# Performance work log

Hardware: AMD Instinct MI355X
Metric: run time of the kernel (lower is better)

Reference implementation:

```python
import jax, jax.numpy as jnp
import numpy as np
from jax import lax

UNITS_OSC = 512
STEPS = 100
DT = 0.001
ACTION_DIM = 256
BATCH = 256


def complex_dense(zc, Wr, Wi, br, bi):
    # zc: [B, 2n] = concat(real, imag); complex matmul with relu on both parts
    n = Wr.shape[0]
    xr, xi = zc[:, :n], zc[:, n:]
    yr = jax.nn.relu(xr @ Wr - xi @ Wi + br)
    yi = jax.nn.relu(xr @ Wi + xi @ Wr + bi)
    return jnp.concatenate([yr, yi], axis=-1)


def hopf_step(zc, omega, mu, b):
    # zc: [B, 2*UNITS_OSC]; Hopf dynamics dz = ((mu - |z|^2) + i*k*omega) z + b, Euler step
    x, y = zc[:, :UNITS_OSC], zc[:, UNITS_OSC:]
    r2 = x * x + y * y
    w = omega * jnp.arange(1, UNITS_OSC + 1, dtype=zc.dtype)  # [B, UNITS_OSC]
    nx = x + DT * ((mu - r2) * x - w * y + b)
    ny = y + DT * ((mu - r2) * y + w * x)
    return jnp.concatenate([nx, ny], axis=-1)


def _dense_init(key, fan_in, fan_out):
    return jax.random.normal(key, (fan_in, fan_out), dtype=jnp.float32) / np.sqrt(fan_in)


def setup_inputs() -> dict:
    key = jax.random.key(0)
    ks = jax.random.split(key, 16)
    inp = {
        'motion_state': jax.random.normal(ks[0], (BATCH, 64), dtype=jnp.float32),
        'robot_state': jax.random.normal(ks[1], (BATCH, 128), dtype=jnp.float32),
        'z': 0.1 * jax.random.normal(ks[2], (BATCH, 2 * UNITS_OSC), dtype=jnp.float32),
        'W_ms': _dense_init(ks[3], 64, 256), 'b_ms': jnp.zeros((256,), jnp.float32),
        'W_rs': _dense_init(ks[4], 128, 256), 'b_rs': jnp.zeros((256,), jnp.float32),
        'W_cmb': _dense_init(ks[5], 512, 512), 'b_cmb': jnp.zeros((512,), jnp.float32),
        'W_om': _dense_init(ks[6], 512, 1), 'b_om': jnp.zeros((1,), jnp.float32),
        'W_mu': _dense_init(ks[7], 512, 512), 'b_mu': jnp.zeros((512,), jnp.float32),
        'W_b': _dense_init(ks[8], 512, 512), 'b_b': jnp.zeros((512,), jnp.float32),
        'Wr0': _dense_init(ks[9], 512, 1024), 'Wi0': _dense_init(ks[10], 512, 1024),
        'br0': jnp.zeros((1024,), jnp.float32), 'bi0': jnp.zeros((1024,), jnp.float32),
        'Wr1': _dense_init(ks[11], 1024, 512), 'Wi1': _dense_init(ks[12], 1024, 512),
        'br1': jnp.zeros((512,), jnp.float32), 'bi1': jnp.zeros((512,), jnp.float32),
        'Wr2': _dense_init(ks[13], 512, 256), 'Wi2': _dense_init(ks[14], 512, 256),
        'br2': jnp.zeros((256,), jnp.float32), 'bi2': jnp.zeros((256,), jnp.float32),
    }
    return inp


def reference(motion_state, robot_state, z,
              W_ms, b_ms, W_rs, b_rs, W_cmb, b_cmb, W_om, b_om, W_mu, b_mu, W_b, b_b,
              Wr0, Wi0, br0, bi0, Wr1, Wi1, br1, bi1, Wr2, Wi2, br2, bi2):
    # --- StateEncoder ---
    ms = jax.nn.relu(motion_state @ W_ms + b_ms)
    rs = jax.nn.relu(robot_state @ W_rs + b_rs)
    st = jax.nn.relu(jnp.concatenate([ms, rs], axis=-1) @ W_cmb + b_cmb)
    omega = jnp.abs(jax.nn.relu(st @ W_om + b_om))   # [B, 1]
    mu = jnp.abs(jax.nn.relu(st @ W_mu + b_mu))      # [B, UNITS_OSC]
    bb = jnp.abs(jax.nn.relu(st @ W_b + b_b))        # [B, UNITS_OSC]

    def mlp(zc):
        zc = complex_dense(zc, Wr0, Wi0, br0, bi0)
        zc = complex_dense(zc, Wr1, Wi1, br1, bi1)
        return complex_dense(zc, Wr2, Wi2, br2, bi2)  # [B, 2*ACTION_DIM]

    # first oscillator step (this z is the z_out returned by the original module)
    z_out = hopf_step(z, omega, mu, bb)
    o0 = mlp(z_out)

    def body(zc, _):
        zn = hopf_step(zc, omega, mu, bb)
        return zn, mlp(zn)

    _, os = lax.scan(body, z_out, None, length=STEPS - 1)   # [STEPS-1, B, 2A]
    out = jnp.concatenate([o0[None], os], axis=0)           # [STEPS, B, 2A]
    out = jnp.transpose(out, (1, 0, 2))[:, :, :ACTION_DIM]  # [B, STEPS, A]
    return out, z_out, omega, mu, bb
```

## Files before the change

### kernel.cpp

```cpp
#include <hip/hip_runtime.h>
#include <hip/hip_bf16.h>

#define STEPS 100
#define DTC 0.001f

typedef __attribute__((ext_vector_type(8))) short bf16x8;
typedef __attribute__((ext_vector_type(4))) float f32x4;

__device__ __forceinline__ void gload16(const void* g, void* l) {
  __builtin_amdgcn_global_load_lds(
      (const __attribute__((address_space(1))) void*)g,
      (__attribute__((address_space(3))) void*)l,
      16, 0, 0);
}


__global__ __launch_bounds__(512)
void front(const float* __restrict__ ms_in, const float* __restrict__ rs_in,
           const float* __restrict__ z,
           const float* __restrict__ Wms, const float* __restrict__ bms,
           const float* __restrict__ Wrs, const float* __restrict__ brs,
           const float* __restrict__ Wc, const float* __restrict__ bc,
           const float* __restrict__ Wmu, const float* __restrict__ bmu,
           const float* __restrict__ Wb, const float* __restrict__ bbias,
           const float* __restrict__ Wom, const float* __restrict__ bom,
           __hip_bfloat16* __restrict__ A0, float* __restrict__ z_out,
           float* __restrict__ om_out, float* __restrict__ mu_out,
           float* __restrict__ bb_out) {
  const int b = blockIdx.x;
  const int n = threadIdx.x;
  __shared__ float sIn[192];
  __shared__ float stA[512];
  __shared__ float stB[512];
  if (n < 64) sIn[n] = ms_in[b * 64 + n];
  else if (n < 192) sIn[n] = rs_in[b * 128 + (n - 64)];
  __syncthreads();
  float a1;
  if (n < 256) {
    a1 = bms[n];
    for (int k = 0; k < 64; ++k) a1 += sIn[k] * Wms[k * 256 + n];
  } else {
    int nn = n - 256;
    a1 = brs[nn];
    for (int k = 0; k < 128; ++k) a1 += sIn[64 + k] * Wrs[k * 256 + nn];
  }
  stA[n] = fmaxf(a1, 0.f);
  __syncthreads();
  float a2 = bc[n];
  for (int k = 0; k < 512; ++k) a2 += stA[k] * Wc[k * 512 + n];
  stB[n] = fmaxf(a2, 0.f);
  __syncthreads();
  float am = bmu[n], ab = bbias[n];
  for (int k = 0; k < 512; ++k) {
    float sv = stB[k];
    am += sv * Wmu[k * 512 + n];
    ab += sv * Wb[k * 512 + n];
  }
  const float muv = fabsf(fmaxf(am, 0.f));
  const float bbv = fabsf(fmaxf(ab, 0.f));
  mu_out[b * 512 + n] = muv;
  bb_out[b * 512 + n] = bbv;
  stA[n] = stB[n] * Wom[n];
  __syncthreads();
  for (int off = 256; off > 0; off >>= 1) {
    if (n < off) stA[n] += stA[n + off];
    __syncthreads();
  }
  const float om = fabsf(fmaxf(stA[0] + bom[0], 0.f));
  if (n == 0) om_out[b] = om;
  float x = z[b * 1024 + n];
  float y = z[b * 1024 + 512 + n];
  const float w = om * (float)(n + 1);
  for (int t = 0; t < STEPS; ++t) {
    float r2 = x * x + y * y;
    float g = muv - r2;
    float nx = x + DTC * (g * x - w * y + bbv);
    float ny = y + DTC * (g * y + w * x);
    x = nx; y = ny;
    if (t == 0) {
      z_out[b * 1024 + n] = x;
      z_out[b * 1024 + 512 + n] = y;
    }
    size_t row = (size_t)b * STEPS + t;
    A0[row * 1024 + n] = __float2bfloat16(x);
    A0[row * 1024 + 512 + n] = __float2bfloat16(y);
  }
}


__constant__ int    jSrcC[10] = {0, 1, 1, 0, 2, 3, 3, 2, 4, 5};
__constant__ float  jSgnC[10] = {1.f, 1.f, -1.f, 1.f, 1.f, 1.f, -1.f, 1.f, 1.f, -1.f};
__constant__ int    jCC[10]   = {1024, 1024, 1024, 1024, 512, 512, 512, 512, 256, 256};
__constant__ int    jDstC[10] = {0, 0, 0, 0, 1, 1, 1, 1, 2, 2};
__constant__ int    jDsC[10]  = {1024, 1024, 1024, 1024, 2048, 2048, 2048, 2048, 1024, 1024};
__constant__ long   jOffC[10] = {0, 1048576, 512, 1049088, 0, 1048576, 1024, 1049600, 0, 512};

__global__ void tpack_all(const float* __restrict__ Wr0, const float* __restrict__ Wi0,
                          const float* __restrict__ Wr1, const float* __restrict__ Wi1,
                          const float* __restrict__ Wr2, const float* __restrict__ Wi2,
                          __hip_bfloat16* __restrict__ BT0, __hip_bfloat16* __restrict__ BT1,
                          __hip_bfloat16* __restrict__ BT2) {
  __shared__ float tile[32][33];
  const int bid = blockIdx.x;
  int j, w;
  if (bid < 4096) { j = bid >> 9; w = bid & 511; }
  else            { j = 8 + ((bid - 4096) >> 7); w = (bid - 4096) & 127; }
  const float* srcs[6] = {Wr0, Wi0, Wr1, Wi1, Wr2, Wi2};
  __hip_bfloat16* dsts[3] = {BT0, BT1, BT2};
  const float* src = srcs[jSrcC[j]];
  __hip_bfloat16* dst = dsts[jDstC[j]] + jOffC[j];
  const int C = jCC[j], ds = jDsC[j];
  const float sign = jSgnC[j];
  const int ncb = C >> 5;
  const int cb = (w % ncb) * 32, rb = (w / ncb) * 32;
  const int tx = threadIdx.x, ty = threadIdx.y;
#pragma unroll
  for (int i = 0; i < 32; i += 8)
    tile[ty + i][tx] = src[(size_t)(rb + ty + i) * C + (cb + tx)];
  __syncthreads();
#pragma unroll
  for (int i = 0; i < 32; i += 8)
    dst[(size_t)(cb + ty + i) * ds + (rb + tx)] = __float2bfloat16(sign * tile[tx][ty + i]);
}


template <int OUT_BF16>
__global__ __launch_bounds__(256)
void gemm_bt(const __hip_bfloat16* __restrict__ A, const __hip_bfloat16* __restrict__ BT,
             const float* __restrict__ biasA, const float* __restrict__ biasB, int bsplit,
             void* __restrict__ Cout, int M, int N, int K) {
  __shared__ __align__(16) __hip_bfloat16 As[128 * 32];
  __shared__ __align__(16) __hip_bfloat16 Bs[128 * 32];
  const int tid = threadIdx.x;
  const int lane = tid & 63;
  const int wid = tid >> 6;
  const int wr = wid >> 1, wc = wid & 1;
  const int fr = lane & 15, fq = lane >> 4;
  const int m0 = blockIdx.y * 128;
  const int n0 = blockIdx.x * 128;

  const __hip_bfloat16* Ag = A + (size_t)(m0 + (tid >> 2)) * K + (tid & 3) * 8;
  const __hip_bfloat16* Ag2 = Ag + (size_t)64 * K;
  const __hip_bfloat16* Bg = BT + (size_t)(n0 + (tid >> 2)) * K + (tid & 3) * 8;
  const __hip_bfloat16* Bg2 = Bg + (size_t)64 * K;
  char* AsB = (char*)&As[0] + wid * 1024;
  char* BsB = (char*)&Bs[0] + wid * 1024;

  f32x4 acc[4][4] = {};

  const int ksteps = K >> 5;
  for (int ks = 0; ks < ksteps; ++ks) {
    __syncthreads();
    gload16(Ag, AsB);
    gload16(Ag2, AsB + 4096);
    gload16(Bg, BsB);
    gload16(Bg2, BsB + 4096);
    Ag += 32; Ag2 += 32; Bg += 32; Bg2 += 32;
    __syncthreads();

    bf16x8 af[4], bfr[4];
#pragma unroll
    for (int i = 0; i < 4; ++i)
      af[i] = *(const bf16x8*)&As[(wr * 64 + i * 16 + fr) * 32 + fq * 8];
#pragma unroll
    for (int j = 0; j < 4; ++j)
      bfr[j] = *(const bf16x8*)&Bs[(wc * 64 + j * 16 + fr) * 32 + fq * 8];
#pragma unroll
    for (int i = 0; i < 4; ++i)
#pragma unroll
      for (int j = 0; j < 4; ++j)
        acc[i][j] = __builtin_amdgcn_mfma_f32_16x16x32_bf16(af[i], bfr[j], acc[i][j], 0, 0, 0);
  }

#pragma unroll
  for (int j = 0; j < 4; ++j) {
    int col = n0 + wc * 64 + j * 16 + fr;
    float bv = (col < bsplit) ? biasA[col] : biasB[col - bsplit];
#pragma unroll
    for (int i = 0; i < 4; ++i) {
#pragma unroll
      for (int r = 0; r < 4; ++r) {
        int row = m0 + wr * 64 + i * 16 + fq * 4 + r;
        float v = fmaxf(acc[i][j][r] + bv, 0.f);
        if (OUT_BF16)
          ((__hip_bfloat16*)Cout)[(size_t)row * N + col] = __float2bfloat16(v);
        else
          ((float*)Cout)[(size_t)row * N + col] = v;
      }
    }
  }
}


#define LOAD_A(DST, a, cb) do { _Pragma("unroll") for (int i = 0; i < 4; ++i) { \
  DST[i][0] = *(const bf16x8*)((cb) + aoff0 + ((a)*4+i)*2048); \
  DST[i][1] = *(const bf16x8*)((cb) + aoff1 + ((a)*4+i)*2048); } } while(0)

#define LOAD_B(b, BF, cb) do { _Pragma("unroll") for (int j = 0; j < 2; ++j) { \
  BF[j][0] = *(const bf16x8*)((cb) + boff0 + ((b)*2+j)*2048); \
  BF[j][1] = *(const bf16x8*)((cb) + boff1 + ((b)*2+j)*2048); } } while(0)

#define MFMA_Q(ASET, a, b, BF) do { _Pragma("unroll") for (int i = 0; i < 4; ++i) \
  _Pragma("unroll") for (int j = 0; j < 2; ++j) { \
    acc[(a)*4+i][(b)*2+j] = __builtin_amdgcn_mfma_f32_16x16x32_bf16(ASET[i][0], BF[j][0], acc[(a)*4+i][(b)*2+j], 0, 0, 0); \
    acc[(a)*4+i][(b)*2+j] = __builtin_amdgcn_mfma_f32_16x16x32_bf16(ASET[i][1], BF[j][1], acc[(a)*4+i][(b)*2+j], 0, 0, 0); } } while(0)

#define SBAR __builtin_amdgcn_sched_barrier(0)

__global__ __launch_bounds__(512, 2)
void gemm256(const __hip_bfloat16* __restrict__ A, const __hip_bfloat16* __restrict__ BT,
             const float* __restrict__ biasA, const float* __restrict__ biasB, int bsplit,
             __hip_bfloat16* __restrict__ Cout, int N, int K, int ntn) {
  extern __shared__ char lds[];

  const int tid = threadIdx.x;
  const int lane = tid & 63;
  const int wid = tid >> 6;
  const int wr = wid >> 2;
  const int wc = wid & 3;
  const int fr = lane & 15, fq = lane >> 4;

  const int nwg = gridDim.x;
  int f = blockIdx.x;
  f = (f & 7) * (nwg >> 3) + (f >> 3);
  const int m0 = (f / ntn) * 256;
  const int n0 = (f % ntn) * 256;

  const int c8v = (tid & 7) ^ ((tid >> 3) & 7);
  const __hip_bfloat16* Asrc0 = A + (size_t)(m0 + (tid >> 3)) * K + c8v * 8;
  const __hip_bfloat16* Asrc1 = Asrc0 + (size_t)128 * K;
  const __hip_bfloat16* Bsrc0 = BT + (size_t)(n0 + (tid >> 3)) * K + c8v * 8;
  const __hip_bfloat16* Bsrc1 = Bsrc0 + (size_t)128 * K;

  const int x0 = fq ^ (fr & 7);
  const int aoff0 = wr * 16384 + fr * 128 + x0 * 16;
  const int aoff1 = wr * 16384 + fr * 128 + (x0 ^ 4) * 16;
  const int boff0 = 32768 + (wc >> 1) * 16384 + ((wc & 1) * 64 + fr) * 128 + x0 * 16;
  const int boff1 = 32768 + (wc >> 1) * 16384 + ((wc & 1) * 64 + fr) * 128 + (x0 ^ 4) * 16;

  auto stage2 = [&](const __hip_bfloat16* base, char* dst) {
    gload16(base, dst + wid * 1024);
    gload16(base + (size_t)64 * K, dst + 8192 + wid * 1024);
  };

  stage2(Asrc0, 0 + lds);
  stage2(Asrc1, lds + 16384);
  stage2(Bsrc0, lds + 32768);
  stage2(Bsrc1, lds + 49152);

  f32x4 acc[8][4] = {};
  bf16x8 af[4][2], ag[4][2], bfA[2][2], bfB[2][2];

  const int nk = K >> 6;
  for (int kt = 0; kt < nk - 1; ++kt) {
    const int cur = kt & 1;
    char* cb = lds + cur * 65536;
    char* nb = lds + (cur ^ 1) * 65536;
    const int ko = (kt + 1) << 6;
    __builtin_amdgcn_s_barrier();
    SBAR;
    stage2(Asrc0 + ko, nb);
    SBAR;
    asm volatile("s_waitcnt vmcnt(2)" ::: "memory");
    __builtin_amdgcn_s_barrier();
    SBAR;
    LOAD_A(af, 0, cb);
    LOAD_B(0, bfA, cb);
    SBAR;
    LOAD_B(1, bfB, cb);
    asm volatile("s_waitcnt lgkmcnt(4)" ::: "memory");
    SBAR;
    __builtin_amdgcn_s_setprio(1); MFMA_Q(af, 0, 0, bfA); __builtin_amdgcn_s_setprio(0);
    __builtin_amdgcn_s_barrier();
    SBAR;
    stage2(Asrc1 + ko, nb + 16384);
    LOAD_A(ag, 1, cb);
    asm volatile("s_waitcnt lgkmcnt(8)" ::: "memory");
    SBAR;
    __builtin_amdgcn_s_setprio(1); MFMA_Q(af, 0, 1, bfB); __builtin_amdgcn_s_setprio(0);
    __builtin_amdgcn_s_barrier();
    SBAR;
    stage2(Bsrc0 + ko, nb + 32768);
    asm volatile("s_waitcnt lgkmcnt(0)" ::: "memory");
    SBAR;
    __builtin_amdgcn_s_setprio(1); MFMA_Q(ag, 1, 1, bfB); __builtin_amdgcn_s_setprio(0);
    __builtin_amdgcn_s_barrier();
    SBAR;
    stage2(Bsrc1 + ko, nb + 49152);
    SBAR;
    __builtin_amdgcn_s_setprio(1); MFMA_Q(ag, 1, 0, bfA); __builtin_amdgcn_s_setprio(0);
  }
  {
    char* cb = lds + ((nk - 1) & 1) * 65536;
    __builtin_amdgcn_s_barrier();
    asm volatile("s_waitcnt vmcnt(0)" ::: "memory");
    __builtin_amdgcn_s_barrier();
    SBAR;
    LOAD_A(af, 0, cb);
    LOAD_B(0, bfA, cb);
    SBAR;
    LOAD_B(1, bfB, cb);
    asm volatile("s_waitcnt lgkmcnt(4)" ::: "memory");
    SBAR;
    __builtin_amdgcn_s_setprio(1); MFMA_Q(af, 0, 0, bfA); __builtin_amdgcn_s_setprio(0);
    LOAD_A(ag, 1, cb);
    asm volatile("s_waitcnt lgkmcnt(8)" ::: "memory");
    SBAR;
    __builtin_amdgcn_s_setprio(1); MFMA_Q(af, 0, 1, bfB); __builtin_amdgcn_s_setprio(0);
    asm volatile("s_waitcnt lgkmcnt(0)" ::: "memory");
    SBAR;
    __builtin_amdgcn_s_setprio(1); MFMA_Q(ag, 1, 1, bfB); MFMA_Q(ag, 1, 0, bfA);
    __builtin_amdgcn_s_setprio(0);
  }

#pragma unroll
  for (int nj = 0; nj < 4; ++nj) {
    const int col = n0 + wc * 64 + nj * 16 + fr;
    const float bv = (col < bsplit) ? biasA[col] : biasB[col - bsplit];
#pragma unroll
    for (int mi = 0; mi < 8; ++mi) {
#pragma unroll
      for (int r = 0; r < 4; ++r) {
        const int row = m0 + wr * 128 + mi * 16 + fq * 4 + r;
        float v = fmaxf(acc[mi][nj][r] + bv, 0.f);
        Cout[(size_t)row * N + col] = __float2bfloat16(v);
      }
    }
  }
}


extern "C" void kernel_launch(void* const* d_in, const int* in_sizes, int n_in,
                              void* d_out, int out_size, void* d_ws, size_t ws_size,
                              hipStream_t stream) {
  const float* motion = (const float*)d_in[0];
  const float* robot  = (const float*)d_in[1];
  const float* z      = (const float*)d_in[2];
  const float* W_ms   = (const float*)d_in[3];
  const float* b_ms   = (const float*)d_in[4];
  const float* W_rs   = (const float*)d_in[5];
  const float* b_rs   = (const float*)d_in[6];
  const float* W_cmb  = (const float*)d_in[7];
  const float* b_cmb  = (const float*)d_in[8];
  const float* W_om   = (const float*)d_in[9];
  const float* b_om   = (const float*)d_in[10];
  const float* W_mu   = (const float*)d_in[11];
  const float* b_mu   = (const float*)d_in[12];
  const float* W_b    = (const float*)d_in[13];
  const float* b_b    = (const float*)d_in[14];
  const float* Wr0    = (const float*)d_in[15];
  const float* Wi0    = (const float*)d_in[16];
  const float* br0    = (const float*)d_in[17];
  const float* bi0    = (const float*)d_in[18];
  const float* Wr1    = (const float*)d_in[19];
  const float* Wi1    = (const float*)d_in[20];
  const float* br1    = (const float*)d_in[21];
  const float* bi1    = (const float*)d_in[22];
  const float* Wr2    = (const float*)d_in[23];
  const float* Wi2    = (const float*)d_in[24];
  const float* br2    = (const float*)d_in[25];

  float* out  = (float*)d_out;
  float* zout = out + (size_t)6553600;
  float* omg  = zout + 262144;
  float* muo  = omg + 256;
  float* bbo  = muo + 131072;

  char* ws = (char*)d_ws;
  __hip_bfloat16* BT0 = (__hip_bfloat16*)ws;
  __hip_bfloat16* BT1 = BT0 + (size_t)2048 * 1024;
  __hip_bfloat16* BT2 = BT1 + (size_t)1024 * 2048;
  __hip_bfloat16* A0  = BT2 + (size_t)256 * 1024;
  __hip_bfloat16* C1  = A0 + (size_t)25600 * 1024;
  __hip_bfloat16* C2  = C1 + (size_t)25600 * 2048;

  front<<<256, 512, 0, stream>>>(motion, robot, z, W_ms, b_ms, W_rs, b_rs,
                                 W_cmb, b_cmb, W_mu, b_mu, W_b, b_b, W_om, b_om,
                                 A0, zout, omg, muo, bbo);

  tpack_all<<<4352, dim3(32, 8), 0, stream>>>(Wr0, Wi0, Wr1, Wi1, Wr2, Wi2,
                                              BT0, BT1, BT2);

  gemm256<<<800, 512, 131072, stream>>>(A0, BT0, br0, bi0, 1024, C1, 2048, 1024, 8);
  gemm256<<<400, 512, 131072, stream>>>(C1, BT1, br1, bi1, 512, C2, 1024, 2048, 4);
  gemm_bt<0><<<dim3(2, 200), 256, 0, stream>>>(C2, BT2, br2, br2, 256, out,
                                               25600, 256, 1024);
}
```

Baseline: 322.6 us.

## Replace 256x256 GEMMs with a 160x128 ping-pong tiled GEMM for all layers

Replaces the 256x256, 512-thread GEMM and the simple 128x128 final-layer GEMM with one templated 160x128 tile kernel (256 threads, two blocks per CU, 72KB LDS). Its double-buffered global-to-LDS staging is interleaved with four MFMA phases. M=25600 divides evenly into 160-row tiles, and the smaller tile gives more workgroups (2560/1280/320), so the CUs should be filled more evenly across waves. The final layer also gains the pipelined path. In exchange, each tile reuses its operands less, so more data must come from global memory and L2.

```diff
diff --git a/kernel.cpp b/kernel.cpp
--- a/kernel.cpp
+++ b/kernel.cpp
@@ -124,206 +124,143 @@
 }
 
 
+#define SBAR __builtin_amdgcn_sched_barrier(0)
+
+#define RD_A(DST, QX, cb) do { _Pragma("unroll") for (int mi = 0; mi < 5; ++mi) \
+  DST[mi] = *(const bf16x8*)((cb) + (abase ^ ((QX) * 64)) + mi * 2048); } while (0)
+
+#define RD_B(DST, h, QX, cb) do { _Pragma("unroll") for (int jj = 0; jj < 2; ++jj) \
+  DST[jj] = *(const bf16x8*)((cb) + (bbase ^ ((QX) * 64)) + (2 * (h) + jj) * 2048); } while (0)
+
+#define MF_PH(ASET, BSET, h) do { _Pragma("unroll") for (int mi = 0; mi < 5; ++mi) \
+  _Pragma("unroll") for (int jj = 0; jj < 2; ++jj) \
+    acc[mi][2 * (h) + jj] = __builtin_amdgcn_mfma_f32_16x16x32_bf16( \
+        ASET[mi], BSET[jj], acc[mi][2 * (h) + jj], 0, 0, 0); } while (0)
+
 template <int OUT_BF16>
-__global__ __launch_bounds__(256)
-void gemm_bt(const __hip_bfloat16* __restrict__ A, const __hip_bfloat16* __restrict__ BT,
+__global__ __launch_bounds__(256, 2)
+void gemm160(const __hip_bfloat16* __restrict__ A, const __hip_bfloat16* __restrict__ BT,
              const float* __restrict__ biasA, const float* __restrict__ biasB, int bsplit,
-             void* __restrict__ Cout, int M, int N, int K) {
-  __shared__ __align__(16) __hip_bfloat16 As[128 * 32];
-  __shared__ __align__(16) __hip_bfloat16 Bs[128 * 32];
+             void* __restrict__ Cout, int N, int K, int ntn_l2) {
+  extern __shared__ char lds[];
+
   const int tid = threadIdx.x;
   const int lane = tid & 63;
   const int wid = tid >> 6;
-  const int wr = wid >> 1, wc = wid & 1;
+  const int wr = wid >> 1;
+  const int wc = wid & 1;
   const int fr = lane & 15, fq = lane >> 4;
-  const int m0 = blockIdx.y * 128;
-  const int n0 = blockIdx.x * 128;
-
-  const __hip_bfloat16* Ag = A + (size_t)(m0 + (tid >> 2)) * K + (tid & 3) * 8;
-  const __hip_bfloat16* Ag2 = Ag + (size_t)64 * K;
-  const __hip_bfloat16* Bg = BT + (size_t)(n0 + (tid >> 2)) * K + (tid & 3) * 8;
-  const __hip_bfloat16* Bg2 = Bg + (size_t)64 * K;
-  char* AsB = (char*)&As[0] + wid * 1024;
-  char* BsB = (char*)&Bs[0] + wid * 1024;
-
-  f32x4 acc[4][4] = {};
-
-  const int ksteps = K >> 5;
-  for (int ks = 0; ks < ksteps; ++ks) {
-    __syncthreads();
-    gload16(Ag, AsB);
-    gload16(Ag2, AsB + 4096);
-    gload16(Bg, BsB);
-    gload16(Bg2, BsB + 4096);
-    Ag += 32; Ag2 += 32; Bg += 32; Bg2 += 32;
-    __syncthreads();
-
-    bf16x8 af[4], bfr[4];
-#pragma unroll
-    for (int i = 0; i < 4; ++i)
-      af[i] = *(const bf16x8*)&As[(wr * 64 + i * 16 + fr) * 32 + fq * 8];
-#pragma unroll
-    for (int j = 0; j < 4; ++j)
-      bfr[j] = *(const bf16x8*)&Bs[(wc * 64 + j * 16 + fr) * 32 + fq * 8];
-#pragma unroll
-    for (int i = 0; i < 4; ++i)
-#pragma unroll
-      for (int j = 0; j < 4; ++j)
-        acc[i][j] = __builtin_amdgcn_mfma_f32_16x16x32_bf16(af[i], bfr[j], acc[i][j], 0, 0, 0);
-  }
-
-#pragma unroll
-  for (int j = 0; j < 4; ++j) {
-    int col = n0 + wc * 64 + j * 16 + fr;
-    float bv = (col < bsplit) ? biasA[col] : biasB[col - bsplit];
-#pragma unroll
-    for (int i = 0; i < 4; ++i) {
+
+  const int nwg = gridDim.x;
+  int f = blockIdx.x;
+  f = (f & 7) * (nwg >> 3) + (f >> 3);
+  const int m0 = (f >> ntn_l2) * 160;
+  const int n0 = (f & ((1 << ntn_l2) - 1)) << 7;
+
+  const int rA = tid >> 3;
+  const int c8v = (tid & 7) ^ (rA & 7);
+  const __hip_bfloat16* Asrc = A + (size_t)(m0 + rA) * K + c8v * 8;
+  const __hip_bfloat16* Bsrc = BT + (size_t)(n0 + rA) * K + c8v * 8;
+
+  const int x0 = fq ^ (fr & 7);
+  const int abase = (wr * 80 + fr) * 128 + x0 * 16;
+  const int bbase = 20480 + (wc * 64 + fr) * 128 + x0 * 16;
+
+  auto stgA = [&](int j, int ko, char* buf) {
+    gload16(Asrc + ko + (size_t)32 * j * K, buf + j * 4096 + wid * 1024);
+  };
+  auto stgB = [&](int j, int ko, char* buf) {
+    gload16(Bsrc + ko + (size_t)32 * j * K, buf + 20480 + j * 4096 + wid * 1024);
+  };
+
+  stgA(0, 0, lds); stgA(1, 0, lds); stgA(2, 0, lds); stgA(3, 0, lds); stgA(4, 0, lds);
+  stgB(0, 0, lds); stgB(1, 0, lds); stgB(2, 0, lds); stgB(3, 0, lds);
+
+  f32x4 acc[5][4] = {};
+  bf16x8 a0[5], a1[5], b00[2], b10[2], b01[2], b11[2];
+
+  const int nk = K >> 6;
+  for (int kt = 0; kt < nk - 1; ++kt) {
+    char* cb = lds + (kt & 1) * 36864;
+    char* nb = lds + ((kt & 1) ^ 1) * 36864;
+    const int ko = (kt + 1) << 6;
+    __builtin_amdgcn_s_barrier();
+    SBAR;
+    stgA(0, ko, nb); stgA(1, ko, nb);
+    SBAR;
+    asm volatile("s_waitcnt vmcnt(2)" ::: "memory");
+    __builtin_amdgcn_s_barrier();
+    SBAR;
+    RD_A(a0, 0, cb);
+    RD_B(b00, 0, 0, cb);
+    SBAR;
+    RD_B(b10, 1, 0, cb);
+    asm volatile("s_waitcnt lgkmcnt(2)" ::: "memory");
+    SBAR;
+    __builtin_amdgcn_s_setprio(1); MF_PH(a0, b00, 0); __builtin_amdgcn_s_setprio(0);
+    __builtin_amdgcn_s_barrier();
+    SBAR;
+    stgA(2, ko, nb); stgA(3, ko, nb); stgA(4, ko, nb);
+    RD_A(a1, 1, cb);
+    RD_B(b01, 0, 1, cb);
+    asm volatile("s_waitcnt lgkmcnt(7)" ::: "memory");
+    SBAR;
+    __builtin_amdgcn_s_setprio(1); MF_PH(a0, b10, 1); __builtin_amdgcn_s_setprio(0);
+    __builtin_amdgcn_s_barrier();
+    SBAR;
+    stgB(0, ko, nb); stgB(1, ko, nb);
+    RD_B(b11, 1, 1, cb);
+    asm volatile("s_waitcnt lgkmcnt(2)" ::: "memory");
+    SBAR;
+    __builtin_amdgcn_s_setprio(1); MF_PH(a1, b01, 0); __builtin_amdgcn_s_setprio(0);
+    __builtin_amdgcn_s_barrier();
+    SBAR;
+    stgB(2, ko, nb); stgB(3, ko, nb);
+    asm volatile("s_waitcnt lgkmcnt(0)" ::: "memory");
+    SBAR;
+    __builtin_amdgcn_s_setprio(1); MF_PH(a1, b11, 1); __builtin_amdgcn_s_setprio(0);
+  }
+  {
+    char* cb = lds + ((nk - 1) & 1) * 36864;
+    __builtin_amdgcn_s_barrier();
+    asm volatile("s_waitcnt vmcnt(0)" ::: "memory");
+    __builtin_amdgcn_s_barrier();
+    SBAR;
+    RD_A(a0, 0, cb);
+    RD_B(b00, 0, 0, cb);
+    SBAR;
+    RD_B(b10, 1, 0, cb);
+    asm volatile("s_waitcnt lgkmcnt(2)" ::: "memory");
+    SBAR;
+    __builtin_amdgcn_s_setprio(1); MF_PH(a0, b00, 0); __builtin_amdgcn_s_setprio(0);
+    RD_A(a1, 1, cb);
+    RD_B(b01, 0, 1, cb);
+    asm volatile("s_waitcnt lgkmcnt(7)" ::: "memory");
+    SBAR;
+    __builtin_amdgcn_s_setprio(1); MF_PH(a0, b10, 1); __builtin_amdgcn_s_setprio(0);
+    RD_B(b11, 1, 1, cb);
+    asm volatile("s_waitcnt lgkmcnt(2)" ::: "memory");
+    SBAR;
+    __builtin_amdgcn_s_setprio(1); MF_PH(a1, b01, 0); __builtin_amdgcn_s_setprio(0);
+    asm volatile("s_waitcnt lgkmcnt(0)" ::: "memory");
+    SBAR;
+    __builtin_amdgcn_s_setprio(1); MF_PH(a1, b11, 1); __builtin_amdgcn_s_setprio(0);
+  }
+
+#pragma unroll
+  for (int nj = 0; nj < 4; ++nj) {
+    const int col = n0 + wc * 64 + nj * 16 + fr;
+    const float bv = (col < bsplit) ? biasA[col] : biasB[col - bsplit];
+#pragma unroll
+    for (int mi = 0; mi < 5; ++mi) {
 #pragma unroll
       for (int r = 0; r < 4; ++r) {
-        int row = m0 + wr * 64 + i * 16 + fq * 4 + r;
-        float v = fmaxf(acc[i][j][r] + bv, 0.f);
+        const int row = m0 + wr * 80 + mi * 16 + fq * 4 + r;
+        float v = fmaxf(acc[mi][nj][r] + bv, 0.f);
         if (OUT_BF16)
           ((__hip_bfloat16*)Cout)[(size_t)row * N + col] = __float2bfloat16(v);
         else
           ((float*)Cout)[(size_t)row * N + col] = v;
-      }
-    }
-  }
-}
-
-
-#define LOAD_A(DST, a, cb) do { _Pragma("unroll") for (int i = 0; i < 4; ++i) { \
-  DST[i][0] = *(const bf16x8*)((cb) + aoff0 + ((a)*4+i)*2048); \
-  DST[i][1] = *(const bf16x8*)((cb) + aoff1 + ((a)*4+i)*2048); } } while(0)
-
-#define LOAD_B(b, BF, cb) do { _Pragma("unroll") for (int j = 0; j < 2; ++j) { \
-  BF[j][0] = *(const bf16x8*)((cb) + boff0 + ((b)*2+j)*2048); \
-  BF[j][1] = *(const bf16x8*)((cb) + boff1 + ((b)*2+j)*2048); } } while(0)
-
-#define MFMA_Q(ASET, a, b, BF) do { _Pragma("unroll") for (int i = 0; i < 4; ++i) \
-  _Pragma("unroll") for (int j = 0; j < 2; ++j) { \
-    acc[(a)*4+i][(b)*2+j] = __builtin_amdgcn_mfma_f32_16x16x32_bf16(ASET[i][0], BF[j][0], acc[(a)*4+i][(b)*2+j], 0, 0, 0); \
-    acc[(a)*4+i][(b)*2+j] = __builtin_amdgcn_mfma_f32_16x16x32_bf16(ASET[i][1], BF[j][1], acc[(a)*4+i][(b)*2+j], 0, 0, 0); } } while(0)
-
-#define SBAR __builtin_amdgcn_sched_barrier(0)
-
-__global__ __launch_bounds__(512, 2)
-void gemm256(const __hip_bfloat16* __restrict__ A, const __hip_bfloat16* __restrict__ BT,
-             const float* __restrict__ biasA, const float* __restrict__ biasB, int bsplit,
-             __hip_bfloat16* __restrict__ Cout, int N, int K, int ntn) {
-  extern __shared__ char lds[];
-
-  const int tid = threadIdx.x;
-  const int lane = tid & 63;
-  const int wid = tid >> 6;
-  const int wr = wid >> 2;
-  const int wc = wid & 3;
-  const int fr = lane & 15, fq = lane >> 4;
-
-  const int nwg = gridDim.x;
-  int f = blockIdx.x;
-  f = (f & 7) * (nwg >> 3) + (f >> 3);
-  const int m0 = (f / ntn) * 256;
-  const int n0 = (f % ntn) * 256;
-
-  const int c8v = (tid & 7) ^ ((tid >> 3) & 7);
-  const __hip_bfloat16* Asrc0 = A + (size_t)(m0 + (tid >> 3)) * K + c8v * 8;
-  const __hip_bfloat16* Asrc1 = Asrc0 + (size_t)128 * K;
-  const __hip_bfloat16* Bsrc0 = BT + (size_t)(n0 + (tid >> 3)) * K + c8v * 8;
-  const __hip_bfloat16* Bsrc1 = Bsrc0 + (size_t)128 * K;
-
-  const int x0 = fq ^ (fr & 7);
-  const int aoff0 = wr * 16384 + fr * 128 + x0 * 16;
-  const int aoff1 = wr * 16384 + fr * 128 + (x0 ^ 4) * 16;
-  const int boff0 = 32768 + (wc >> 1) * 16384 + ((wc & 1) * 64 + fr) * 128 + x0 * 16;
-  const int boff1 = 32768 + (wc >> 1) * 16384 + ((wc & 1) * 64 + fr) * 128 + (x0 ^ 4) * 16;
-
-  auto stage2 = [&](const __hip_bfloat16* base, char* dst) {
-    gload16(base, dst + wid * 1024);
-    gload16(base + (size_t)64 * K, dst + 8192 + wid * 1024);
-  };
-
-  stage2(Asrc0, 0 + lds);
-  stage2(Asrc1, lds + 16384);
-  stage2(Bsrc0, lds + 32768);
-  stage2(Bsrc1, lds + 49152);
-
-  f32x4 acc[8][4] = {};
-  bf16x8 af[4][2], ag[4][2], bfA[2][2], bfB[2][2];
-
-  const int nk = K >> 6;
-  for (int kt = 0; kt < nk - 1; ++kt) {
-    const int cur = kt & 1;
-    char* cb = lds + cur * 65536;
-    char* nb = lds + (cur ^ 1) * 65536;
-    const int ko = (kt + 1) << 6;
-    __builtin_amdgcn_s_barrier();
-    SBAR;
-    stage2(Asrc0 + ko, nb);
-    SBAR;
-    asm volatile("s_waitcnt vmcnt(2)" ::: "memory");
-    __builtin_amdgcn_s_barrier();
-    SBAR;
-    LOAD_A(af, 0, cb);
-    LOAD_B(0, bfA, cb);
-    SBAR;
-    LOAD_B(1, bfB, cb);
-    asm volatile("s_waitcnt lgkmcnt(4)" ::: "memory");
-    SBAR;
-    __builtin_amdgcn_s_setprio(1); MFMA_Q(af, 0, 0, bfA); __builtin_amdgcn_s_setprio(0);
-    __builtin_amdgcn_s_barrier();
-    SBAR;
-    stage2(Asrc1 + ko, nb + 16384);
-    LOAD_A(ag, 1, cb);
-    asm volatile("s_waitcnt lgkmcnt(8)" ::: "memory");
-    SBAR;
-    __builtin_amdgcn_s_setprio(1); MFMA_Q(af, 0, 1, bfB); __builtin_amdgcn_s_setprio(0);
-    __builtin_amdgcn_s_barrier();
-    SBAR;
-    stage2(Bsrc0 + ko, nb + 32768);
-    asm volatile("s_waitcnt lgkmcnt(0)" ::: "memory");
-    SBAR;
-    __builtin_amdgcn_s_setprio(1); MFMA_Q(ag, 1, 1, bfB); __builtin_amdgcn_s_setprio(0);
-    __builtin_amdgcn_s_barrier();
-    SBAR;
-    stage2(Bsrc1 + ko, nb + 49152);
-    SBAR;
-    __builtin_amdgcn_s_setprio(1); MFMA_Q(ag, 1, 0, bfA); __builtin_amdgcn_s_setprio(0);
-  }
-  {
-    char* cb = lds + ((nk - 1) & 1) * 65536;
-    __builtin_amdgcn_s_barrier();
-    asm volatile("s_waitcnt vmcnt(0)" ::: "memory");
-    __builtin_amdgcn_s_barrier();
-    SBAR;
-    LOAD_A(af, 0, cb);
-    LOAD_B(0, bfA, cb);
-    SBAR;
-    LOAD_B(1, bfB, cb);
-    asm volatile("s_waitcnt lgkmcnt(4)" ::: "memory");
-    SBAR;
-    __builtin_amdgcn_s_setprio(1); MFMA_Q(af, 0, 0, bfA); __builtin_amdgcn_s_setprio(0);
-    LOAD_A(ag, 1, cb);
-    asm volatile("s_waitcnt lgkmcnt(8)" ::: "memory");
-    SBAR;
-    __builtin_amdgcn_s_setprio(1); MFMA_Q(af, 0, 1, bfB); __builtin_amdgcn_s_setprio(0);
-    asm volatile("s_waitcnt lgkmcnt(0)" ::: "memory");
-    SBAR;
-    __builtin_amdgcn_s_setprio(1); MFMA_Q(ag, 1, 1, bfB); MFMA_Q(ag, 1, 0, bfA);
-    __builtin_amdgcn_s_setprio(0);
-  }
-
-#pragma unroll
-  for (int nj = 0; nj < 4; ++nj) {
-    const int col = n0 + wc * 64 + nj * 16 + fr;
-    const float bv = (col < bsplit) ? biasA[col] : biasB[col - bsplit];
-#pragma unroll
-    for (int mi = 0; mi < 8; ++mi) {
-#pragma unroll
-      for (int r = 0; r < 4; ++r) {
-        const int row = m0 + wr * 128 + mi * 16 + fq * 4 + r;
-        float v = fmaxf(acc[mi][nj][r] + bv, 0.f);
-        Cout[(size_t)row * N + col] = __float2bfloat16(v);
       }
     }
   }
@@ -381,8 +318,7 @@
   tpack_all<<<4352, dim3(32, 8), 0, stream>>>(Wr0, Wi0, Wr1, Wi1, Wr2, Wi2,
                                               BT0, BT1, BT2);
 
-  gemm256<<<800, 512, 131072, stream>>>(A0, BT0, br0, bi0, 1024, C1, 2048, 1024, 8);
-  gemm256<<<400, 512, 131072, stream>>>(C1, BT1, br1, bi1, 512, C2, 1024, 2048, 4);
-  gemm_bt<0><<<dim3(2, 200), 256, 0, stream>>>(C2, BT2, br2, br2, 256, out,
-                                               25600, 256, 1024);
-}
+  gemm160<1><<<2560, 256, 73728, stream>>>(A0, BT0, br0, bi0, 1024, C1, 2048, 1024, 4);
+  gemm160<1><<<1280, 256, 73728, stream>>>(C1, BT1, br1, bi1, 512, C2, 1024, 2048, 3);
+  gemm160<0><<<320, 256, 73728, stream>>>(C2, BT2, br2, br2, 256, out, 256, 1024, 1);
+}
```

New measurement: 298.5 us. 7.5% less time.
